# Kernel tuning notes

Hardware: AMD Instinct MI355X
Metric: run time of the kernel (lower is better)

## Reference

```python
import jax, jax.numpy as jnp
import numpy as np

B, S, H = 2, 2048, 2048
NH, NKV = 16, 4
HD = H // NH            # 128
GROUPS = NH // NKV      # 4
ROTARY_BASE = 10000.0
NEG = -1e9


def setup_inputs() -> dict:
    key = jax.random.key(0)
    ks = jax.random.split(key, 6)
    x = jax.random.normal(ks[0], (B, S, H), dtype=jnp.float32)
    # additive causal mask [B,1,S,S]
    causal = jnp.where(jnp.tril(jnp.ones((S, S), dtype=bool)), 0.0, NEG).astype(jnp.float32)
    attention_mask = jnp.broadcast_to(causal[None, None], (B, 1, S, S))
    position_ids = jnp.broadcast_to(jnp.arange(S, dtype=jnp.int32)[None], (B, S))
    sc = 0.02
    Wq = jax.random.normal(ks[1], (H, NH * HD), dtype=jnp.float32) * sc
    Wk = jax.random.normal(ks[2], (H, NKV * HD), dtype=jnp.float32) * sc
    Wv = jax.random.normal(ks[3], (H, NKV * HD), dtype=jnp.float32) * sc
    Wo = jax.random.normal(ks[4], (H, H), dtype=jnp.float32) * sc
    return {"x": x, "attention_mask": attention_mask, "position_ids": position_ids,
            "Wq": Wq, "Wk": Wk, "Wv": Wv, "Wo": Wo}


def _rotate_half(t):
    t1, t2 = t[..., : HD // 2], t[..., HD // 2:]
    return jnp.concatenate((-t2, t1), axis=-1)


def _rope_sin_cos(position_ids, dtype):
    inv_freq = 1.0 / (ROTARY_BASE ** (jnp.arange(0, HD, 2, dtype=jnp.float32) / HD))  # [HD/2]
    freqs = position_ids.astype(jnp.float32)[..., None] * inv_freq[None, None, :]      # [B,S,HD/2]
    emb = jnp.concatenate((freqs, freqs), axis=-1)                                     # [B,S,HD]
    return jnp.sin(emb).astype(dtype), jnp.cos(emb).astype(dtype)


def reference(x, attention_mask, position_ids, Wq, Wk, Wv, Wo):
    # QKV projections (no bias)
    q = (x @ Wq).reshape(B, S, NH, HD).transpose(0, 2, 1, 3)     # [B,NH,S,HD]
    k = (x @ Wk).reshape(B, S, NKV, HD).transpose(0, 2, 1, 3)    # [B,NKV,S,HD]
    v = (x @ Wv).reshape(B, S, NKV, HD).transpose(0, 2, 1, 3)
    sin, cos = _rope_sin_cos(position_ids, x.dtype)
    sin, cos = sin[:, None], cos[:, None]                         # unsqueeze head dim
    q = q * cos + _rotate_half(q) * sin
    k = k * cos + _rotate_half(k) * sin
    # GQA: repeat kv heads
    k = jnp.repeat(k, GROUPS, axis=1)                             # [B,NH,S,HD]
    v = jnp.repeat(v, GROUPS, axis=1)
    scores = jnp.einsum('bhqd,bhkd->bhqk', q, k) / jnp.sqrt(jnp.asarray(HD, x.dtype))
    scores = scores + attention_mask                              # additive causal mask
    attn = jax.nn.softmax(scores.astype(jnp.float32), axis=-1).astype(x.dtype)
    # dropout p=0.0 -> no-op
    out = jnp.einsum('bhqk,bhkd->bhqd', attn, v)                  # [B,NH,S,HD]
    out = out.transpose(0, 2, 1, 3).reshape(B, S, H)
    return out @ Wo
```

## Files before the change

kernel.cpp:

```cpp
#include <hip/hip_runtime.h>
#include <hip/hip_bf16.h>
#include <stdint.h>
#include <math.h>

#define B_ 2
#define S_ 2048
#define H_ 2048
#define NH_ 16
#define NKV_ 4
#define HD_ 128

typedef __bf16 bf16;
typedef __bf16 bf16x8 __attribute__((ext_vector_type(8)));
typedef __bf16 bf16x4 __attribute__((ext_vector_type(4)));
typedef float f32x4 __attribute__((ext_vector_type(4)));

__device__ __forceinline__ void async_copy16(const void* g, void* l) {
  __builtin_amdgcn_global_load_lds(
      (const __attribute__((address_space(1))) void*)(uintptr_t)g,
      (__attribute__((address_space(3))) void*)(uintptr_t)l,
      16, 0, 0);
}

__device__ __forceinline__ f32x4 mfma16(bf16x8 a, bf16x8 b, f32x4 c) {
  return __builtin_amdgcn_mfma_f32_16x16x32_bf16(a, b, c, 0, 0, 0);
}


__global__ void prep_all_k(const float* __restrict__ x,
                           const float* __restrict__ Wq, const float* __restrict__ Wk,
                           const float* __restrict__ Wv, const float* __restrict__ Wo,
                           bf16* __restrict__ xb, bf16* __restrict__ WqkvT,
                           bf16* __restrict__ WoT, float2* __restrict__ tab) {
  __shared__ float tile[32][33];
  const int bid = blockIdx.x;
  const int tid = threadIdx.x;

  if (bid < 10240) {
    const float* W; bf16* Wt; int N, bx, by;
    if (bid < 4096)      { W = Wq; Wt = WqkvT;                       N = 2048; int b2 = bid;        bx = b2 & 63; by = b2 >> 6; }
    else if (bid < 5120) { W = Wk; Wt = WqkvT + (size_t)2048 * 2048; N = 512;  int b2 = bid - 4096; bx = b2 & 15; by = b2 >> 4; }
    else if (bid < 6144) { W = Wv; Wt = WqkvT + (size_t)2560 * 2048; N = 512;  int b2 = bid - 5120; bx = b2 & 15; by = b2 >> 4; }
    else                 { W = Wo; Wt = WoT;                         N = 2048; int b2 = bid - 6144; bx = b2 & 63; by = b2 >> 6; }
    const int K = 2048;
    int n0 = bx * 32, k0 = by * 32;
    int tx = tid & 31, ty = tid >> 5;
#pragma unroll
    for (int j = 0; j < 32; j += 8)
      tile[ty + j][tx] = W[(size_t)(k0 + ty + j) * N + n0 + tx];
    __syncthreads();
#pragma unroll
    for (int j = 0; j < 32; j += 8)
      Wt[(size_t)(n0 + ty + j) * K + k0 + tx] = (bf16)tile[tx][ty + j];
  } else if (bid < 18432) {
    int i = ((bid - 10240) * 256 + tid) * 4;
    float4 v = *(const float4*)(x + i);
    bf16x4 r;
    r[0] = (bf16)v.x; r[1] = (bf16)v.y; r[2] = (bf16)v.z; r[3] = (bf16)v.w;
    *(bf16x4*)(xb + i) = r;
  } else {
    int i = (bid - 18432) * 256 + tid;
    int p = i >> 6, d = i & 63;
    float invf = expf(-((float)(2 * d) / 128.0f) * 9.210340371976184f);
    float fr = (float)p * invf;
    float sv, cv;
    sincosf(fr, &sv, &cv);
    tab[i] = make_float2(cv, sv);
  }
}

__global__ void rope_both_k(bf16* __restrict__ bq, bf16* __restrict__ bk,
                            const int* __restrict__ pos_ids,
                            const float2* __restrict__ tab) {
  int bid = blockIdx.x;
  bf16* t; int hshift, hmask, i; float scale;
  if (bid < 2048) { t = bq; hshift = 4; hmask = 15; scale = 0.12753102f; i = bid * 256 + threadIdx.x; }
  else            { t = bk; hshift = 2; hmask = 3;  scale = 1.0f;        i = (bid - 2048) * 256 + threadIdx.x; }
  int g = i & 7;
  int tmp = i >> 3;
  int h = tmp & hmask;
  int row = tmp >> hshift;
  int pos = pos_ids[row];
  size_t base = (((size_t)row << hshift) + h) * HD_ + g * 8;
  const float2* tb = tab + pos * 64 + g * 8;
  bf16x8 lo = *(const bf16x8*)(t + base);
  bf16x8 hi = *(const bf16x8*)(t + base + 64);
  float4 t0 = *(const float4*)(tb);
  float4 t1 = *(const float4*)(tb + 2);
  float4 t2 = *(const float4*)(tb + 4);
  float4 t3 = *(const float4*)(tb + 6);
  float cs[8], sn[8];
  cs[0]=t0.x; sn[0]=t0.y; cs[1]=t0.z; sn[1]=t0.w;
  cs[2]=t1.x; sn[2]=t1.y; cs[3]=t1.z; sn[3]=t1.w;
  cs[4]=t2.x; sn[4]=t2.y; cs[5]=t2.z; sn[5]=t2.w;
  cs[6]=t3.x; sn[6]=t3.y; cs[7]=t3.z; sn[7]=t3.w;
  bf16x8 olo, ohi;
#pragma unroll
  for (int j = 0; j < 8; ++j) {
    float a = (float)lo[j], b = (float)hi[j];
    olo[j] = (bf16)((a * cs[j] - b * sn[j]) * scale);
    ohi[j] = (bf16)((b * cs[j] + a * sn[j]) * scale);
  }
  *(bf16x8*)(t + base) = olo;
  *(bf16x8*)(t + base + 64) = ohi;
}


template <int MODE, int NJ>
__global__ __launch_bounds__(512) void gemm256_k(const bf16* __restrict__ A,
                                                 const bf16* __restrict__ Bt,
                                                 void* __restrict__ C0,
                                                 void* __restrict__ C1,
                                                 void* __restrict__ C2,
                                                 int M, int N, int K) {
  extern __shared__ __align__(16) char smem[];
  constexpr int BUFSZ = 32768 + NJ * 8192;
  const int tid = threadIdx.x;
  const int lane = tid & 63;
  const int w = tid >> 6;
  const int wm = w >> 2;
  const int wn = w & 3;
  const int g16 = lane >> 4, c16 = lane & 15;
  const int row0 = blockIdx.y * 256;
  const int col0 = blockIdx.x * (NJ * 64);
  const int srow = tid >> 3;
  const int sslot = tid & 7;
  const int ldsw = w * 1024;

  auto stage = [&](int buf, int kt, int r) {
    int rr = (r < 4) ? r : r - 4;
    int row = rr * 64 + srow;
    int ss = sslot ^ (row & 7);
    const bf16* src = (r < 4) ? (A + (size_t)(row0 + row) * K)
                              : (Bt + (size_t)(col0 + row) * K);
    async_copy16(src + (kt << 6) + ss * 8,
                 smem + buf * BUFSZ + ((r < 4) ? 0 : 32768) + rr * 8192 + ldsw);
  };

  int offA[2][8], offB[2][NJ];
#pragma unroll
  for (int ks = 0; ks < 2; ++ks) {
#pragma unroll
    for (int i = 0; i < 8; ++i) {
      int ra = wm * 128 + i * 16 + c16;
      offA[ks][i] = ra * 128 + (((ks * 4 + g16) ^ (ra & 7)) << 4);
    }
#pragma unroll
    for (int j = 0; j < NJ; ++j) {
      int rb = wn * (16 * NJ) + j * 16 + c16;
      offB[ks][j] = 32768 + rb * 128 + (((ks * 4 + g16) ^ (rb & 7)) << 4);
    }
  }

  const f32x4 fz = {0.f, 0.f, 0.f, 0.f};
  f32x4 acc[8][NJ];
#pragma unroll
  for (int i = 0; i < 8; ++i)
#pragma unroll
    for (int j = 0; j < NJ; ++j) acc[i][j] = fz;

  const int nkt = K >> 6;
#pragma unroll
  for (int r = 0; r < 4 + NJ; ++r) stage(0, 0, r);
  asm volatile("s_waitcnt vmcnt(0)" ::: "memory");
  __builtin_amdgcn_s_barrier();

  for (int t = 0; t < nkt; ++t) {
    const char* Ab = smem + (t & 1) * BUFSZ;
    const bool pf = (t + 1 < nkt);
    const int nb = (t + 1) & 1;
    bf16x8 bfr[2][NJ];

    {
      bf16x8 af[2][2];
#pragma unroll
      for (int ks = 0; ks < 2; ++ks) {
#pragma unroll
        for (int j = 0; j < NJ; ++j) bfr[ks][j] = *(const bf16x8*)(Ab + offB[ks][j]);
        af[ks][0] = *(const bf16x8*)(Ab + offA[ks][0]);
        af[ks][1] = *(const bf16x8*)(Ab + offA[ks][1]);
      }
      if (pf) { stage(nb, t + 1, 0); stage(nb, t + 1, 1); stage(nb, t + 1, 2); stage(nb, t + 1, 3); }
      __builtin_amdgcn_s_barrier();
      asm volatile("s_waitcnt lgkmcnt(0)" ::: "memory");
      __builtin_amdgcn_sched_barrier(0);
      __builtin_amdgcn_s_setprio(1);
#pragma unroll
      for (int ks = 0; ks < 2; ++ks)
#pragma unroll
        for (int m = 0; m < 2; ++m)
#pragma unroll
          for (int j = 0; j < NJ; ++j)
            acc[m][j] = mfma16(af[ks][m], bfr[ks][j], acc[m][j]);
      __builtin_amdgcn_s_setprio(0);
      __builtin_amdgcn_sched_barrier(0);
      __builtin_amdgcn_s_barrier();
    }

#pragma unroll
    for (int q = 1; q < 4; ++q) {
      bf16x8 af[2][2];
#pragma unroll
      for (int ks = 0; ks < 2; ++ks) {
        af[ks][0] = *(const bf16x8*)(Ab + offA[ks][q * 2]);
        af[ks][1] = *(const bf16x8*)(Ab + offA[ks][q * 2 + 1]);
      }
      if (q == 1 && pf) {
#pragma unroll
        for (int r = 0; r < NJ; ++r) stage(nb, t + 1, 4 + r);
      }
      __builtin_amdgcn_s_barrier();
      asm volatile("s_waitcnt lgkmcnt(0)" ::: "memory");
      __builtin_amdgcn_sched_barrier(0);
      __builtin_amdgcn_s_setprio(1);
#pragma unroll
      for (int ks = 0; ks < 2; ++ks)
#pragma unroll
        for (int m = 0; m < 2; ++m)
#pragma unroll
          for (int j = 0; j < NJ; ++j)
            acc[q * 2 + m][j] = mfma16(af[ks][m], bfr[ks][j], acc[q * 2 + m][j]);
      __builtin_amdgcn_s_setprio(0);
      __builtin_amdgcn_sched_barrier(0);
      if (q == 3 && pf) asm volatile("s_waitcnt vmcnt(0)" ::: "memory");
      __builtin_amdgcn_s_barrier();
    }
  }

#pragma unroll
  for (int i = 0; i < 8; ++i) {
    int gr0 = row0 + wm * 128 + i * 16 + g16 * 4;
#pragma unroll
    for (int j = 0; j < NJ; ++j) {
      int gc = col0 + wn * (16 * NJ) + j * 16 + c16;
      if constexpr (MODE == 2) {
        if (gc < 2048) {
#pragma unroll
          for (int r = 0; r < 4; ++r)
            ((bf16*)C0)[(size_t)(gr0 + r) * 2048 + gc] = (bf16)acc[i][j][r];
        } else if (gc < 2560) {
#pragma unroll
          for (int r = 0; r < 4; ++r)
            ((bf16*)C1)[(size_t)(gr0 + r) * 512 + (gc - 2048)] = (bf16)acc[i][j][r];
        } else {
          int dv = gc - 2560;
          int hkv = dv >> 7, d = dv & 127;
          size_t va = (((size_t)(gr0 >> 11) * NKV_ + hkv) * HD_ + d) * S_ + (gr0 & 2047);
          bf16x4 pk;
#pragma unroll
          for (int r = 0; r < 4; ++r) pk[r] = (bf16)acc[i][j][r];
          *(bf16x4*)((bf16*)C2 + va) = pk;
        }
      } else {
#pragma unroll
        for (int r = 0; r < 4; ++r) {
          if constexpr (MODE == 1)
            ((float*)C0)[(size_t)(gr0 + r) * N + gc] = acc[i][j][r];
          else
            ((bf16*)C0)[(size_t)(gr0 + r) * N + gc] = (bf16)acc[i][j][r];
        }
      }
    }
  }
}


__global__ __launch_bounds__(256, 2) void attn_fwd_k(const bf16* __restrict__ Qg,
                                                     const bf16* __restrict__ Kg,
                                                     const bf16* __restrict__ VTg,
                                                     bf16* __restrict__ Og) {
  __shared__ __align__(16) bf16 Ks[2][64 * 128];
  __shared__ __align__(16) bf16 Vt[2][128 * 64];

  const int tid = threadIdx.x;
  const int lane = tid & 63;
  const int w = tid >> 6;
  const int g16 = lane >> 4;
  const int c16 = lane & 15;

  const int bid = blockIdx.x;
  const int xcd = bid & 7;
  const int slot = bid >> 3;
  const int v = slot >> 1;
  const int heavy = (((slot & 1) ^ (slot >> 5)) & 1) == 0;
  const int qh = (v & 15) >> 1;
  const int qb = heavy ? (15 - qh) : qh;
  const int hh = ((v & 1) << 1) | (v >> 4);
  const int b = xcd >> 2;
  const int hkv = xcd & 3;
  const int h = hkv * 4 + hh;
  const int q0 = qb * 128;
  const int qw = q0 + w * 32;

  int kfo[4][4];
#pragma unroll
  for (int ksq = 0; ksq < 4; ++ksq)
#pragma unroll
    for (int mt = 0; mt < 4; ++mt) {
      int gp = c16 >> 2, rp = c16 & 3;
      int blk = 8 * (mt >> 1) + 2 * gp + ((mt & 1) ^ (gp & 1));
      int row = blk * 4 + rp;
      kfo[ksq][mt] = row * 256 + (((ksq * 4 + g16) ^ (row & 7)) << 4);
    }
  int vfo[2][8];
#pragma unroll
  for (int ks = 0; ks < 2; ++ks)
#pragma unroll
    for (int dt = 0; dt < 8; ++dt) {
      int rv = dt * 16 + c16;
      vfo[ks][dt] = rv * 128 + (((ks * 4 + g16) ^ (rv & 7)) << 4);
    }

  int koff[4], voff[4];
#pragma unroll
  for (int rd = 0; rd < 4; ++rd) {
    int Lb = rd * 256 + w * 64;
    int rowk = (Lb + lane) >> 4;
    koff[rd] = rowk * (NKV_ * HD_) + (((lane & 15) ^ (rowk & 7)) * 8);
    int rowv = (Lb + lane) >> 3;
    voff[rd] = rowv * S_ + (((lane & 7) ^ (rowv & 7)) * 8);
  }

  bf16x8 qf[2][4];
#pragma unroll
  for (int nq = 0; nq < 2; ++nq)
#pragma unroll
    for (int ksq = 0; ksq < 4; ++ksq)
      qf[nq][ksq] = *(const bf16x8*)(Qg + ((size_t)(b * S_ + qw + nq * 16 + c16) * NH_ + h) * HD_ + (ksq * 4 + g16) * 8);

  float m_run[2] = {-1e30f, -1e30f};
  float l_run[2] = {0.f, 0.f};
  const f32x4 fz = {0.f, 0.f, 0.f, 0.f};
  f32x4 acc[2][8];
#pragma unroll
  for (int nq = 0; nq < 2; ++nq)
#pragma unroll
    for (int dt = 0; dt < 8; ++dt) acc[nq][dt] = fz;

  const bf16* __restrict__ Kgb = Kg + ((size_t)b * S_ * NKV_ + hkv) * HD_;
  const bf16* __restrict__ Vgb = VTg + ((size_t)(b * NKV_ + hkv)) * HD_ * S_;

  auto stage = [&](int buf, int kv0) {
    const bf16* kp = Kgb + (size_t)kv0 * (NKV_ * HD_);
    const bf16* vp = Vgb + kv0;
#pragma unroll
    for (int rd = 0; rd < 4; ++rd)
      async_copy16(kp + koff[rd], (char*)&Ks[buf][0] + (rd * 256 + w * 64) * 16);
#pragma unroll
    for (int rd = 0; rd < 4; ++rd)
      async_copy16(vp + voff[rd], (char*)&Vt[buf][0] + (rd * 256 + w * 64) * 16);
  };

  const int ntiles = 2 * qb + 2;
  stage(0, 0);
  int cur = 0;

  for (int t = 0; t < ntiles; ++t) {
    __syncthreads();
    if (t + 1 < ntiles) stage(cur ^ 1, (t + 1) * 64);
    const int kv0 = t * 64;

    if (kv0 <= qw + 31) {
      const char* KsC = (const char*)&Ks[cur][0];
      const char* VtC = (const char*)&Vt[cur][0];

      f32x4 sc[2][4];
#pragma unroll
      for (int nq = 0; nq < 2; ++nq)
#pragma unroll
        for (int mt = 0; mt < 4; ++mt) sc[nq][mt] = fz;

      __builtin_amdgcn_s_setprio(1);
#pragma unroll
      for (int ksq = 0; ksq < 4; ++ksq) {
        bf16x8 kf[4];
#pragma unroll
        for (int mt = 0; mt < 4; ++mt)
          kf[mt] = *(const bf16x8*)(KsC + kfo[ksq][mt]);
#pragma unroll
        for (int nq = 0; nq < 2; ++nq)
#pragma unroll
          for (int mt = 0; mt < 4; ++mt)
            sc[nq][mt] = mfma16(kf[mt], qf[nq][ksq], sc[nq][mt]);
      }
      __builtin_amdgcn_s_setprio(0);

      if (kv0 + 63 > qw) {
#pragma unroll
        for (int nq = 0; nq < 2; ++nq) {
          int qa = qw + nq * 16 + c16;
#pragma unroll
          for (int mt = 0; mt < 4; ++mt) {
            int blk = 8 * (mt >> 1) + 2 * g16 + ((mt & 1) ^ (g16 & 1));
#pragma unroll
            for (int r = 0; r < 4; ++r) {
              int ka = kv0 + blk * 4 + r;
              if (ka > qa) sc[nq][mt][r] = -1e30f;
            }
          }
        }
      }

      float mx[2];
#pragma unroll
      for (int nq = 0; nq < 2; ++nq) {
        float vv = sc[nq][0][0];
#pragma unroll
        for (int mt = 0; mt < 4; ++mt)
#pragma unroll
          for (int r = 0; r < 4; ++r) vv = fmaxf(vv, sc[nq][mt][r]);
        vv = fmaxf(vv, __shfl_xor(vv, 16));
        vv = fmaxf(vv, __shfl_xor(vv, 32));
        mx[nq] = vv;
      }
      if (__any((mx[0] > m_run[0] + 8.f) || (mx[1] > m_run[1] + 8.f))) {
#pragma unroll
        for (int nq = 0; nq < 2; ++nq) {
          float mn = fmaxf(m_run[nq], mx[nq]);
          float corr = exp2f(m_run[nq] - mn);
          m_run[nq] = mn;
          l_run[nq] *= corr;
#pragma unroll
          for (int dt = 0; dt < 8; ++dt) acc[nq][dt] *= corr;
        }
      }
#pragma unroll
      for (int nq = 0; nq < 2; ++nq) {
        float sum = 0.f;
#pragma unroll
        for (int mt = 0; mt < 4; ++mt)
#pragma unroll
          for (int r = 0; r < 4; ++r) {
            float p = exp2f(sc[nq][mt][r] - m_run[nq]);
            sc[nq][mt][r] = p;
            sum += p;
          }
        sum += __shfl_xor(sum, 16);
        sum += __shfl_xor(sum, 32);
        l_run[nq] += sum;
      }

      bf16x8 pa[2][2];
#pragma unroll
      for (int nq = 0; nq < 2; ++nq)
#pragma unroll
        for (int ks = 0; ks < 2; ++ks) {
          f32x4 sA = (g16 & 1) ? sc[nq][2 * ks + 1] : sc[nq][2 * ks];
          f32x4 sB = (g16 & 1) ? sc[nq][2 * ks] : sc[nq][2 * ks + 1];
          bf16x8 tf;
          tf[0] = (bf16)sA[0]; tf[1] = (bf16)sA[1]; tf[2] = (bf16)sA[2]; tf[3] = (bf16)sA[3];
          tf[4] = (bf16)sB[0]; tf[5] = (bf16)sB[1]; tf[6] = (bf16)sB[2]; tf[7] = (bf16)sB[3];
          pa[nq][ks] = tf;
        }

      __builtin_amdgcn_s_setprio(1);
#pragma unroll
      for (int ks = 0; ks < 2; ++ks)
#pragma unroll
        for (int dt = 0; dt < 8; ++dt) {
          bf16x8 vf = *(const bf16x8*)(VtC + vfo[ks][dt]);
          acc[0][dt] = mfma16(vf, pa[0][ks], acc[0][dt]);
          acc[1][dt] = mfma16(vf, pa[1][ks], acc[1][dt]);
        }
      __builtin_amdgcn_s_setprio(0);
    }
    cur ^= 1;
  }

#pragma unroll
  for (int nq = 0; nq < 2; ++nq) {
    float inv = 1.0f / l_run[nq];
    size_t base = ((size_t)(b * S_ + qw + nq * 16 + c16) * NH_ + h) * HD_ + g16 * 4;
#pragma unroll
    for (int dt = 0; dt < 8; ++dt) {
      bf16x4 ov;
#pragma unroll
      for (int r = 0; r < 4; ++r) ov[r] = (bf16)(acc[nq][dt][r] * inv);
      *(bf16x4*)(Og + base + dt * 16) = ov;
    }
  }
}


extern "C" void kernel_launch(void* const* d_in, const int* in_sizes, int n_in,
                              void* d_out, int out_size, void* d_ws, size_t ws_size,
                              hipStream_t stream) {
  const float* x  = (const float*)d_in[0];
  const int* pos  = (const int*)d_in[2];
  const float* Wq = (const float*)d_in[3];
  const float* Wk = (const float*)d_in[4];
  const float* Wv = (const float*)d_in[5];
  const float* Wo = (const float*)d_in[6];

  char* ws = (char*)d_ws;
  size_t off = 0;
  auto alloc = [&](size_t bytes) -> char* {
    char* p = ws + off;
    off += (bytes + 255) & ~(size_t)255;
    return p;
  };
  const size_t rows = (size_t)B_ * S_;
  bf16* xb    = (bf16*)alloc(rows * H_ * 2);
  bf16* bq    = (bf16*)alloc(rows * (NH_ * HD_) * 2);
  bf16* batt  = (bf16*)alloc(rows * (NH_ * HD_) * 2);
  bf16* WqkvT = (bf16*)alloc((size_t)3072 * H_ * 2);
  bf16* WoT   = (bf16*)alloc((size_t)H_ * H_ * 2);
  bf16* bk    = (bf16*)alloc(rows * (NKV_ * HD_) * 2);
  bf16* VT    = (bf16*)alloc(rows * (NKV_ * HD_) * 2);
  float2* tab = (float2*)alloc((size_t)S_ * 64 * sizeof(float2));

  auto* fqkv = gemm256_k<2, 3>;
  auto* fo   = gemm256_k<1, 2>;
  const int ldsQKV = 2 * (32768 + 3 * 8192);
  const int ldsO   = 2 * (32768 + 2 * 8192);
  (void)hipFuncSetAttribute((const void*)fqkv, hipFuncAttributeMaxDynamicSharedMemorySize, ldsQKV);
  (void)hipFuncSetAttribute((const void*)fo, hipFuncAttributeMaxDynamicSharedMemorySize, ldsO);

  prep_all_k<<<18944, 256, 0, stream>>>(x, Wq, Wk, Wv, Wo, xb, WqkvT, WoT, tab);

  gemm256_k<2, 3><<<dim3(16, 16), 512, ldsQKV, stream>>>(xb, WqkvT, bq, bk, VT, 4096, 3072, 2048);

  rope_both_k<<<2560, 256, 0, stream>>>(bq, bk, pos, tab);

  attn_fwd_k<<<dim3(512), 256, 0, stream>>>(bq, bk, VT, batt);

  gemm256_k<1, 2><<<dim3(16, 16), 512, ldsO, stream>>>(batt, WoT, d_out, nullptr, nullptr, 4096, 2048, 2048);
}
```

Baseline: 195.5 us.

## Halve attention query tile, read V directly from global, raise occupancy

The attention kernel now gives each block 64 query rows (16 per wave) instead of 128, doubling the grid to 1024 blocks and raising launch bounds to 4 blocks per CU. The V tile is no longer staged into LDS; V fragments are loaded straight from global memory inside the PV loop, halving LDS use. Block-to-work mapping is changed to interleave heavy and light causal tiles. The goal is more occupancy and parallelism, at the cost of more K reloads per query and uncached global V loads with worse latency hiding.

```diff
diff --git a/kernel.cpp b/kernel.cpp
--- a/kernel.cpp
+++ b/kernel.cpp
@@ -265,12 +265,11 @@
 }
 
 
-__global__ __launch_bounds__(256, 2) void attn_fwd_k(const bf16* __restrict__ Qg,
+__global__ __launch_bounds__(256, 4) void attn_fwd_k(const bf16* __restrict__ Qg,
                                                      const bf16* __restrict__ Kg,
                                                      const bf16* __restrict__ VTg,
                                                      bf16* __restrict__ Og) {
   __shared__ __align__(16) bf16 Ks[2][64 * 128];
-  __shared__ __align__(16) bf16 Vt[2][128 * 64];
 
   const int tid = threadIdx.x;
   const int lane = tid & 63;
@@ -281,16 +280,14 @@
   const int bid = blockIdx.x;
   const int xcd = bid & 7;
   const int slot = bid >> 3;
-  const int v = slot >> 1;
-  const int heavy = (((slot & 1) ^ (slot >> 5)) & 1) == 0;
-  const int qh = (v & 15) >> 1;
-  const int qb = heavy ? (15 - qh) : qh;
-  const int hh = ((v & 1) << 1) | (v >> 4);
+  const int hh = slot & 3;
+  const int idx = slot >> 2;
+  const int q64 = (idx & 1) ? (idx >> 1) : (31 - (idx >> 1));
   const int b = xcd >> 2;
   const int hkv = xcd & 3;
   const int h = hkv * 4 + hh;
-  const int q0 = qb * 128;
-  const int qw = q0 + w * 32;
+  const int q0 = q64 * 64;
+  const int qw = q0 + w * 16;
 
   int kfo[4][4];
 #pragma unroll
@@ -302,56 +299,40 @@
       int row = blk * 4 + rp;
       kfo[ksq][mt] = row * 256 + (((ksq * 4 + g16) ^ (row & 7)) << 4);
     }
-  int vfo[2][8];
-#pragma unroll
-  for (int ks = 0; ks < 2; ++ks)
-#pragma unroll
-    for (int dt = 0; dt < 8; ++dt) {
-      int rv = dt * 16 + c16;
-      vfo[ks][dt] = rv * 128 + (((ks * 4 + g16) ^ (rv & 7)) << 4);
-    }
-
-  int koff[4], voff[4];
+  int koff[4];
 #pragma unroll
   for (int rd = 0; rd < 4; ++rd) {
-    int Lb = rd * 256 + w * 64;
-    int rowk = (Lb + lane) >> 4;
+    int rowk = (rd * 256 + w * 64 + lane) >> 4;
     koff[rd] = rowk * (NKV_ * HD_) + (((lane & 15) ^ (rowk & 7)) * 8);
-    int rowv = (Lb + lane) >> 3;
-    voff[rd] = rowv * S_ + (((lane & 7) ^ (rowv & 7)) * 8);
-  }
-
-  bf16x8 qf[2][4];
-#pragma unroll
-  for (int nq = 0; nq < 2; ++nq)
-#pragma unroll
-    for (int ksq = 0; ksq < 4; ++ksq)
-      qf[nq][ksq] = *(const bf16x8*)(Qg + ((size_t)(b * S_ + qw + nq * 16 + c16) * NH_ + h) * HD_ + (ksq * 4 + g16) * 8);
-
-  float m_run[2] = {-1e30f, -1e30f};
-  float l_run[2] = {0.f, 0.f};
+  }
+  int voffd[8];
+#pragma unroll
+  for (int dt = 0; dt < 8; ++dt)
+    voffd[dt] = (dt * 16 + c16) * S_ + g16 * 8;
+
+  bf16x8 qf[4];
+#pragma unroll
+  for (int ksq = 0; ksq < 4; ++ksq)
+    qf[ksq] = *(const bf16x8*)(Qg + ((size_t)(b * S_ + qw + c16) * NH_ + h) * HD_ + (ksq * 4 + g16) * 8);
+
+  float m_run = -1e30f;
+  float l_run = 0.f;
   const f32x4 fz = {0.f, 0.f, 0.f, 0.f};
-  f32x4 acc[2][8];
-#pragma unroll
-  for (int nq = 0; nq < 2; ++nq)
-#pragma unroll
-    for (int dt = 0; dt < 8; ++dt) acc[nq][dt] = fz;
+  f32x4 acc[8];
+#pragma unroll
+  for (int dt = 0; dt < 8; ++dt) acc[dt] = fz;
 
   const bf16* __restrict__ Kgb = Kg + ((size_t)b * S_ * NKV_ + hkv) * HD_;
   const bf16* __restrict__ Vgb = VTg + ((size_t)(b * NKV_ + hkv)) * HD_ * S_;
 
   auto stage = [&](int buf, int kv0) {
     const bf16* kp = Kgb + (size_t)kv0 * (NKV_ * HD_);
-    const bf16* vp = Vgb + kv0;
 #pragma unroll
     for (int rd = 0; rd < 4; ++rd)
       async_copy16(kp + koff[rd], (char*)&Ks[buf][0] + (rd * 256 + w * 64) * 16);
-#pragma unroll
-    for (int rd = 0; rd < 4; ++rd)
-      async_copy16(vp + voff[rd], (char*)&Vt[buf][0] + (rd * 256 + w * 64) * 16);
   };
 
-  const int ntiles = 2 * qb + 2;
+  const int ntiles = q64 + 1;
   stage(0, 0);
   int cur = 0;
 
@@ -360,15 +341,12 @@
     if (t + 1 < ntiles) stage(cur ^ 1, (t + 1) * 64);
     const int kv0 = t * 64;
 
-    if (kv0 <= qw + 31) {
+    if (kv0 <= qw + 15) {
       const char* KsC = (const char*)&Ks[cur][0];
-      const char* VtC = (const char*)&Vt[cur][0];
-
-      f32x4 sc[2][4];
-#pragma unroll
-      for (int nq = 0; nq < 2; ++nq)
-#pragma unroll
-        for (int mt = 0; mt < 4; ++mt) sc[nq][mt] = fz;
+
+      f32x4 sc[4];
+#pragma unroll
+      for (int mt = 0; mt < 4; ++mt) sc[mt] = fz;
 
       __builtin_amdgcn_s_setprio(1);
 #pragma unroll
@@ -378,106 +356,84 @@
         for (int mt = 0; mt < 4; ++mt)
           kf[mt] = *(const bf16x8*)(KsC + kfo[ksq][mt]);
 #pragma unroll
-        for (int nq = 0; nq < 2; ++nq)
-#pragma unroll
-          for (int mt = 0; mt < 4; ++mt)
-            sc[nq][mt] = mfma16(kf[mt], qf[nq][ksq], sc[nq][mt]);
+        for (int mt = 0; mt < 4; ++mt)
+          sc[mt] = mfma16(kf[mt], qf[ksq], sc[mt]);
       }
       __builtin_amdgcn_s_setprio(0);
 
       if (kv0 + 63 > qw) {
-#pragma unroll
-        for (int nq = 0; nq < 2; ++nq) {
-          int qa = qw + nq * 16 + c16;
-#pragma unroll
-          for (int mt = 0; mt < 4; ++mt) {
-            int blk = 8 * (mt >> 1) + 2 * g16 + ((mt & 1) ^ (g16 & 1));
-#pragma unroll
-            for (int r = 0; r < 4; ++r) {
-              int ka = kv0 + blk * 4 + r;
-              if (ka > qa) sc[nq][mt][r] = -1e30f;
-            }
+        int qa = qw + c16;
+#pragma unroll
+        for (int mt = 0; mt < 4; ++mt) {
+          int blk = 8 * (mt >> 1) + 2 * g16 + ((mt & 1) ^ (g16 & 1));
+#pragma unroll
+          for (int r = 0; r < 4; ++r) {
+            int ka = kv0 + blk * 4 + r;
+            if (ka > qa) sc[mt][r] = -1e30f;
           }
         }
       }
 
-      float mx[2];
-#pragma unroll
-      for (int nq = 0; nq < 2; ++nq) {
-        float vv = sc[nq][0][0];
-#pragma unroll
-        for (int mt = 0; mt < 4; ++mt)
-#pragma unroll
-          for (int r = 0; r < 4; ++r) vv = fmaxf(vv, sc[nq][mt][r]);
-        vv = fmaxf(vv, __shfl_xor(vv, 16));
-        vv = fmaxf(vv, __shfl_xor(vv, 32));
-        mx[nq] = vv;
-      }
-      if (__any((mx[0] > m_run[0] + 8.f) || (mx[1] > m_run[1] + 8.f))) {
-#pragma unroll
-        for (int nq = 0; nq < 2; ++nq) {
-          float mn = fmaxf(m_run[nq], mx[nq]);
-          float corr = exp2f(m_run[nq] - mn);
-          m_run[nq] = mn;
-          l_run[nq] *= corr;
-#pragma unroll
-          for (int dt = 0; dt < 8; ++dt) acc[nq][dt] *= corr;
+      float mx = sc[0][0];
+#pragma unroll
+      for (int mt = 0; mt < 4; ++mt)
+#pragma unroll
+        for (int r = 0; r < 4; ++r) mx = fmaxf(mx, sc[mt][r]);
+      mx = fmaxf(mx, __shfl_xor(mx, 16));
+      mx = fmaxf(mx, __shfl_xor(mx, 32));
+      if (__any(mx > m_run + 8.f)) {
+        float mn = fmaxf(m_run, mx);
+        float corr = exp2f(m_run - mn);
+        m_run = mn;
+        l_run *= corr;
+#pragma unroll
+        for (int dt = 0; dt < 8; ++dt) acc[dt] *= corr;
+      }
+      float sum = 0.f;
+#pragma unroll
+      for (int mt = 0; mt < 4; ++mt)
+#pragma unroll
+        for (int r = 0; r < 4; ++r) {
+          float p = exp2f(sc[mt][r] - m_run);
+          sc[mt][r] = p;
+          sum += p;
         }
-      }
-#pragma unroll
-      for (int nq = 0; nq < 2; ++nq) {
-        float sum = 0.f;
-#pragma unroll
-        for (int mt = 0; mt < 4; ++mt)
-#pragma unroll
-          for (int r = 0; r < 4; ++r) {
-            float p = exp2f(sc[nq][mt][r] - m_run[nq]);
-            sc[nq][mt][r] = p;
-            sum += p;
-          }
-        sum += __shfl_xor(sum, 16);
-        sum += __shfl_xor(sum, 32);
-        l_run[nq] += sum;
-      }
-
-      bf16x8 pa[2][2];
-#pragma unroll
-      for (int nq = 0; nq < 2; ++nq)
-#pragma unroll
-        for (int ks = 0; ks < 2; ++ks) {
-          f32x4 sA = (g16 & 1) ? sc[nq][2 * ks + 1] : sc[nq][2 * ks];
-          f32x4 sB = (g16 & 1) ? sc[nq][2 * ks] : sc[nq][2 * ks + 1];
-          bf16x8 tf;
-          tf[0] = (bf16)sA[0]; tf[1] = (bf16)sA[1]; tf[2] = (bf16)sA[2]; tf[3] = (bf16)sA[3];
-          tf[4] = (bf16)sB[0]; tf[5] = (bf16)sB[1]; tf[6] = (bf16)sB[2]; tf[7] = (bf16)sB[3];
-          pa[nq][ks] = tf;
-        }
+      sum += __shfl_xor(sum, 16);
+      sum += __shfl_xor(sum, 32);
+      l_run += sum;
+
+      bf16x8 pa[2];
+#pragma unroll
+      for (int ks = 0; ks < 2; ++ks) {
+        f32x4 sA = (g16 & 1) ? sc[2 * ks + 1] : sc[2 * ks];
+        f32x4 sB = (g16 & 1) ? sc[2 * ks] : sc[2 * ks + 1];
+        bf16x8 tf;
+        tf[0] = (bf16)sA[0]; tf[1] = (bf16)sA[1]; tf[2] = (bf16)sA[2]; tf[3] = (bf16)sA[3];
+        tf[4] = (bf16)sB[0]; tf[5] = (bf16)sB[1]; tf[6] = (bf16)sB[2]; tf[7] = (bf16)sB[3];
+        pa[ks] = tf;
+      }
 
       __builtin_amdgcn_s_setprio(1);
 #pragma unroll
       for (int ks = 0; ks < 2; ++ks)
 #pragma unroll
         for (int dt = 0; dt < 8; ++dt) {
-          bf16x8 vf = *(const bf16x8*)(VtC + vfo[ks][dt]);
-          acc[0][dt] = mfma16(vf, pa[0][ks], acc[0][dt]);
-          acc[1][dt] = mfma16(vf, pa[1][ks], acc[1][dt]);
+          bf16x8 vf = *(const bf16x8*)(Vgb + voffd[dt] + kv0 + ks * 32);
+          acc[dt] = mfma16(vf, pa[ks], acc[dt]);
         }
       __builtin_amdgcn_s_setprio(0);
     }
     cur ^= 1;
   }
 
-#pragma unroll
-  for (int nq = 0; nq < 2; ++nq) {
-    float inv = 1.0f / l_run[nq];
-    size_t base = ((size_t)(b * S_ + qw + nq * 16 + c16) * NH_ + h) * HD_ + g16 * 4;
-#pragma unroll
-    for (int dt = 0; dt < 8; ++dt) {
-      bf16x4 ov;
-#pragma unroll
-      for (int r = 0; r < 4; ++r) ov[r] = (bf16)(acc[nq][dt][r] * inv);
-      *(bf16x4*)(Og + base + dt * 16) = ov;
-    }
+  float inv = 1.0f / l_run;
+  size_t base = ((size_t)(b * S_ + qw + c16) * NH_ + h) * HD_ + g16 * 4;
+#pragma unroll
+  for (int dt = 0; dt < 8; ++dt) {
+    bf16x4 ov;
+#pragma unroll
+    for (int r = 0; r < 4; ++r) ov[r] = (bf16)(acc[dt][r] * inv);
+    *(bf16x4*)(Og + base + dt * 16) = ov;
   }
 }
 
@@ -522,7 +478,7 @@
 
   rope_both_k<<<2560, 256, 0, stream>>>(bq, bk, pos, tab);
 
-  attn_fwd_k<<<dim3(512), 256, 0, stream>>>(bq, bk, VT, batt);
+  attn_fwd_k<<<dim3(1024), 256, 0, stream>>>(bq, bk, VT, batt);
 
   gemm256_k<1, 2><<<dim3(16, 16), 512, ldsO, stream>>>(batt, WoT, d_out, nullptr, nullptr, 4096, 2048, 2048);
 }
```

Result: slower. 329.8 us (+68.7%).
